# Kernel tuning notes

Hardware: AMD Instinct MI355X
Metric: run time of the kernel (lower is better)

The kernel has to match this reference:

```python
import jax, jax.numpy as jnp
import numpy as np

DIM = 192
HEADS = 4
EPS_LN = 1e-5
EPS_NORM = 1e-12


def _layernorm(x, w, b):
    # x: [b, c, h, w]; normalize over channel dim (equiv to 'b (h w) c' LN over last axis)
    mu = jnp.mean(x, axis=1, keepdims=True)
    var = jnp.mean((x - mu) ** 2, axis=1, keepdims=True)
    return (x - mu) / jnp.sqrt(var + EPS_LN) * w[None, :, None, None] + b[None, :, None, None]


def _conv1x1(x, w):
    # w: [out_c, in_c]
    return jnp.einsum('bchw,oc->bohw', x, w)


def _dwconv3x3(x, w):
    # w: [c, 1, 3, 3], depthwise (groups = c), padding 1
    return jax.lax.conv_general_dilated(
        x, w, window_strides=(1, 1), padding='SAME',
        feature_group_count=x.shape[1],
        dimension_numbers=('NCHW', 'OIHW', 'NCHW'))


def _l2norm(x):
    # F.normalize(dim=-1): x / max(||x||_2, eps)
    n = jnp.sqrt(jnp.sum(x * x, axis=-1, keepdims=True))
    return x / jnp.maximum(n, EPS_NORM)


def setup_inputs() -> dict:
    key = jax.random.key(0)
    ks = jax.random.split(key, 10)
    b, c, h, w = 8, DIM, 128, 128
    inp = {
        'xx': jax.random.normal(ks[0], (b, c, h, w), jnp.float32),
        'q_in': jax.random.normal(ks[1], (b, c, h, w), jnp.float32),
        'ln_w': jnp.ones((c,), jnp.float32),
        'ln_b': jnp.zeros((c,), jnp.float32),
        'w_q': jax.random.normal(ks[2], (c, c), jnp.float32) * 0.02,
        'w_k': jax.random.normal(ks[3], (c, c), jnp.float32) * 0.02,
        'w_v': jax.random.normal(ks[4], (c, c), jnp.float32) * 0.02,
        'wd_q': jax.random.normal(ks[5], (c, 1, 3, 3), jnp.float32) * 0.1,
        'wd_k': jax.random.normal(ks[6], (c, 1, 3, 3), jnp.float32) * 0.1,
        'wd_v': jax.random.normal(ks[7], (c, 1, 3, 3), jnp.float32) * 0.1,
        'w_proj': jax.random.normal(ks[8], (c, c), jnp.float32) * 0.02,
        'temperature': jnp.ones((HEADS, 1, 1), jnp.float32),
    }
    return inp


def reference(xx, q_in, ln_w, ln_b, w_q, w_k, w_v, wd_q, wd_k, wd_v, w_proj, temperature):
    b, c, h, w = xx.shape
    hw = h * w
    dh = c // HEADS  # per-head channel dim

    x_n = _layernorm(xx, ln_w, ln_b)
    q_n = _layernorm(q_in, ln_w, ln_b)

    q = _dwconv3x3(_conv1x1(q_n, w_q), wd_q)
    k = _dwconv3x3(_conv1x1(x_n, w_k), wd_k)
    v = _dwconv3x3(_conv1x1(x_n, w_v), wd_v)

    # b (head c) h w -> b head c (h w)
    q = q.reshape(b, HEADS, dh, hw)
    k = k.reshape(b, HEADS, dh, hw)
    v = v.reshape(b, HEADS, dh, hw)

    q = _l2norm(q)
    k = _l2norm(k)

    # channel-channel attention: [b, head, dh, dh]
    attn = jnp.einsum('bhcn,bhdn->bhcd', q, k) * temperature[None]
    attn = jax.nn.softmax(attn, axis=-1)

    out = jnp.einsum('bhcd,bhdn->bhcn', attn, v)  # [b, head, dh, hw]
    out = out.reshape(b, c, h, w)
    out = _conv1x1(out, w_proj) + q_in
    return out
```

## Files before the change

### kernel.cpp

```cpp
#include <hip/hip_runtime.h>
#include <hip/hip_bf16.h>
#include <stdint.h>

#define HWSZ 16384
#define CCH 192
#define NB 8
#define NHEAD 4
#define DHEAD 48

typedef unsigned short u16;
typedef __bf16 bf16x8 __attribute__((ext_vector_type(8)));
typedef float f32x4 __attribute__((ext_vector_type(4)));
typedef short s16x8 __attribute__((ext_vector_type(8)));
typedef short s16x4 __attribute__((ext_vector_type(4)));

__device__ __forceinline__ float b2f(u16 h){
  union { unsigned u; float f; } v; v.u = ((unsigned)h) << 16; return v.f;
}
__device__ __forceinline__ u16 f2b(float f){
  union { float f; unsigned u; } v; v.f = f;
  unsigned r = v.u + 0x7fffu + ((v.u >> 16) & 1u);
  return (u16)(r >> 16);
}

__global__ __launch_bounds__(256) void k_wpack(
    const float* __restrict__ wq, const float* __restrict__ wk,
    const float* __restrict__ wv, u16* __restrict__ o)
{
  int m = blockIdx.x;
  const float* src = (m == 0) ? wq : (m == 1) ? wk : wv;
  u16* dst = o + (size_t)m * CCH * CCH;
  int tid = threadIdx.x;
  #pragma unroll
  for (int i = 0; i < 36; ++i){
    int e = (i * 256 + tid) * 4;
    float4 v = *(const float4*)(src + e);
    s16x4 pk;
    pk[0] = (short)f2b(v.x); pk[1] = (short)f2b(v.y);
    pk[2] = (short)f2b(v.z); pk[3] = (short)f2b(v.w);
    *(s16x4*)(dst + e) = pk;
  }
}

__global__ __launch_bounds__(256) void k_stats(
    const float* __restrict__ xx, const float* __restrict__ q_in,
    float* __restrict__ st)
{
  int tid = threadIdx.x;
  int px  = blockIdx.x * 256 + tid;
  int b   = blockIdx.y, sel = blockIdx.z;
  const float* in = (sel ? q_in : xx) + (size_t)b * CCH * HWSZ + px;
  float s0 = 0.f, s1 = 0.f, q0 = 0.f, q1 = 0.f;
  #pragma unroll 8
  for (int c = 0; c < CCH; c += 2){
    float va = in[(size_t)c * HWSZ];
    float vb = in[(size_t)(c + 1) * HWSZ];
    s0 += va; q0 += va * va;
    s1 += vb; q1 += vb * vb;
  }
  float s = s0 + s1, ss = q0 + q1;
  float mu  = s * (1.f / CCH);
  float var = ss * (1.f / CCH) - mu * mu;
  float2 o = make_float2(mu, rsqrtf(var + 1e-5f));
  *(float2*)(st + ((size_t)(sel * NB + b) * HWSZ + px) * 2) = o;
}

__global__ __launch_bounds__(512) void k_conv(
    const float* __restrict__ xx, const float* __restrict__ q_in,
    const float* __restrict__ St,
    const float* __restrict__ lnw, const float* __restrict__ lnb,
    const u16* __restrict__ Wb,
    u16* __restrict__ Ok, u16* __restrict__ Ov, u16* __restrict__ Oq)
{
  __shared__ u16 lnT[96 * 264];
  int tid = threadIdx.x;
  int b   = blockIdx.y;
  int z   = blockIdx.z;
  int p0  = blockIdx.x * 128;

  {
    const float* xb = (z ? q_in : xx) + (size_t)b * CCH * HWSZ + p0;
    const float* sb = St + ((size_t)(z * NB + b) * HWSZ + p0) * 2;
    #pragma unroll
    for (int i = 0; i < 6; ++i){
      int e = i * 512 + tid;
      int c = e >> 4, ns = (e & 15) * 8;
      float4 v0 = *(const float4*)(xb + (size_t)c * HWSZ + ns);
      float4 v1 = *(const float4*)(xb + (size_t)c * HWSZ + ns + 4);
      float4 t0 = *(const float4*)(sb + ns * 2);
      float4 t1 = *(const float4*)(sb + ns * 2 + 4);
      float4 t2 = *(const float4*)(sb + ns * 2 + 8);
      float4 t3 = *(const float4*)(sb + ns * 2 + 12);
      float lw_ = lnw[c], lb_ = lnb[c];
      s16x8 pk;
      pk[0] = (short)f2b((v0.x - t0.x) * t0.y * lw_ + lb_);
      pk[1] = (short)f2b((v0.y - t0.z) * t0.w * lw_ + lb_);
      pk[2] = (short)f2b((v0.z - t1.x) * t1.y * lw_ + lb_);
      pk[3] = (short)f2b((v0.w - t1.z) * t1.w * lw_ + lb_);
      pk[4] = (short)f2b((v1.x - t2.x) * t2.y * lw_ + lb_);
      pk[5] = (short)f2b((v1.y - t2.z) * t2.w * lw_ + lb_);
      pk[6] = (short)f2b((v1.z - t3.x) * t3.y * lw_ + lb_);
      pk[7] = (short)f2b((v1.w - t3.z) * t3.w * lw_ + lb_);
      int kb   = c >> 5, kr = c & 31;
      int tile = (kr >> 2) & 1;
      int mr   = ((kr >> 3) << 2) | (kr & 3);
      int ti   = (kb * 8 + (ns >> 4)) * 2 + tile;
      *(s16x8*)(&lnT[ti * 264 + mr * 16 + (ns & 15)]) = pk;
    }
  }
  __syncthreads();

  int lane = tid & 63, wid = tid >> 6;
  int quad = lane >> 4, r = lane & 15;
  int mq = wid & 3;
  int wm = mq * 48;
  const u16* W;
  u16* O;
  if (z == 0){
    W = Wb + (size_t)((wid >> 2) + 1) * CCH * CCH;
    O = (wid >> 2) ? Ov : Ok;
  } else {
    W = Wb;
    O = Oq;
  }
  int nt  = z ? 1 : 2;
  int nhS = z ? (wid >> 2) : 0;
  const u16* A0 = W + (size_t)wm * CCH;
  unsigned lvb0 = (unsigned)(uintptr_t)(&lnT[0]) + 2u * (unsigned)(r + quad * 64);
  size_t ob = (size_t)b * CCH * HWSZ;

  for (int t = 0; t < nt; ++t){
    int nh = z ? nhS : t;
    f32x4 acc[3][4] = {};
    bf16x8 aC[3], aN[3];
    #pragma unroll
    for (int i = 0; i < 3; ++i)
      aC[i] = *(const bf16x8*)(A0 + (size_t)(i * 16 + r) * CCH + quad * 8);
    #pragma unroll
    for (int kb = 0; kb < 6; ++kb){
      s16x4 lo[4], hi[4];
      #pragma unroll
      for (int j = 0; j < 4; ++j){
        unsigned a = lvb0 + (unsigned)(kb * 8448 + (nh * 4 + j) * 1056);
        asm volatile("ds_read_b64_tr_b16 %0, %1" : "=&v"(lo[j]) : "v"(a));
        asm volatile("ds_read_b64_tr_b16 %0, %1 offset:528" : "=&v"(hi[j]) : "v"(a));
      }
      if (kb < 5){
        #pragma unroll
        for (int i = 0; i < 3; ++i)
          aN[i] = *(const bf16x8*)(A0 + (size_t)(i * 16 + r) * CCH + (kb + 1) * 32 + quad * 8);
      }
      asm volatile("s_waitcnt lgkmcnt(0)" ::: "memory");
      __builtin_amdgcn_sched_barrier(0);
      #pragma unroll
      for (int j = 0; j < 4; ++j){
        union { s16x8 s; bf16x8 b; } u;
        u.s = __builtin_shufflevector(lo[j], hi[j], 0, 1, 2, 3, 4, 5, 6, 7);
        #pragma unroll
        for (int i = 0; i < 3; ++i)
          acc[i][j] = __builtin_amdgcn_mfma_f32_16x16x32_bf16(aC[i], u.b, acc[i][j], 0, 0, 0);
      }
      #pragma unroll
      for (int i = 0; i < 3; ++i) aC[i] = aN[i];
    }
    #pragma unroll
    for (int i = 0; i < 3; ++i){
      #pragma unroll
      for (int rg = 0; rg < 4; ++rg){
        int o = wm + i * 16 + quad * 4 + rg;
        size_t rowb = ob + (size_t)o * HWSZ;
        #pragma unroll
        for (int j = 0; j < 4; ++j)
          O[rowb + p0 + nh * 64 + j * 16 + r] = f2b(acc[i][j][rg]);
      }
    }
  }
}

__global__ __launch_bounds__(256) void k_dw3(
    const float* __restrict__ wq, const float* __restrict__ wk,
    const float* __restrict__ wv,
    u16* __restrict__ bq, u16* __restrict__ bk, u16* __restrict__ bv,
    float* __restrict__ ssq_q, float* __restrict__ ssq_k)
{
  int tid = threadIdx.x;
  int bc  = blockIdx.x;
  int z   = blockIdx.y;
  int c   = bc % CCH;
  const float* wd = (z == 0) ? wq : (z == 1) ? wk : wv;
  u16* buf = (z == 0) ? bq : (z == 1) ? bk : bv;
  float w[9];
  #pragma unroll
  for (int t = 0; t < 9; ++t) w[t] = wd[c * 9 + t];
  u16* p = buf + (size_t)bc * HWSZ;

  int xseg = tid & 15, ygrp = tid >> 4;
  int x0 = xseg * 8, y0 = ygrp * 8;

  s16x8 zz = {0,0,0,0,0,0,0,0};
  s16x8 raw[10];
  #pragma unroll
  for (int rr = 0; rr < 10; ++rr){
    int yy = y0 - 1 + rr;
    raw[rr] = (yy >= 0 && yy < 128) ? *(const s16x8*)(p + yy * 128 + x0) : zz;
  }
  __syncthreads();

  float cf[10][8];
  float lf[10], rgt[10];
  #pragma unroll
  for (int rr = 0; rr < 10; ++rr){
    #pragma unroll
    for (int j = 0; j < 8; ++j) cf[rr][j] = b2f((u16)raw[rr][j]);
    float l  = __shfl_up(cf[rr][7], 1);
    float rr_ = __shfl_down(cf[rr][0], 1);
    lf[rr]  = (xseg > 0)  ? l   : 0.f;
    rgt[rr] = (xseg < 15) ? rr_ : 0.f;
  }

  float ss = 0.f;
  #pragma unroll
  for (int k = 0; k < 8; ++k){
    float acc[8] = {0.f,0.f,0.f,0.f,0.f,0.f,0.f,0.f};
    #pragma unroll
    for (int dy = 0; dy < 3; ++dy){
      int rr = k + dy;
      float wl = w[dy * 3], wc = w[dy * 3 + 1], wr = w[dy * 3 + 2];
      acc[0] += wl * lf[rr] + wc * cf[rr][0] + wr * cf[rr][1];
      #pragma unroll
      for (int j = 1; j < 7; ++j)
        acc[j] += wl * cf[rr][j - 1] + wc * cf[rr][j] + wr * cf[rr][j + 1];
      acc[7] += wl * cf[rr][6] + wc * cf[rr][7] + wr * rgt[rr];
    }
    s16x8 pk;
    #pragma unroll
    for (int j = 0; j < 8; ++j){
      pk[j] = (short)f2b(acc[j]);
      ss += acc[j] * acc[j];
    }
    *(s16x8*)(p + (y0 + k) * 128 + x0) = pk;
  }

  if (z < 2){
    #pragma unroll
    for (int m = 32; m > 0; m >>= 1) ss += __shfl_xor(ss, m);
    if ((tid & 63) == 0) atomicAdd(&((z == 0) ? ssq_q : ssq_k)[bc], ss);
  }
}

__global__ void k_gram(const u16* __restrict__ q, const u16* __restrict__ k,
                       float* __restrict__ G)
{
  __shared__ float gs[4 * 48 * 49];
  int tid = threadIdx.x;
  int chunk = blockIdx.x;
  int h = blockIdx.y, b = blockIdx.z;
  int lane = tid & 63, w = tid >> 6;
  int quad = lane >> 4, r = lane & 15;
  int nb = chunk * 1024 + w * 256;
  const u16* qb = q + ((size_t)b * CCH + h * DHEAD) * HWSZ;
  const u16* kb = k + ((size_t)b * CCH + h * DHEAD) * HWSZ;
  f32x4 acc[3][3] = {};
  for (int s = 0; s < 8; ++s){
    int kk = nb + s * 32 + quad * 8;
    bf16x8 af[3], bfr[3];
    #pragma unroll
    for (int i = 0; i < 3; ++i){
      af[i]  = *(const bf16x8*)(qb + (size_t)(i * 16 + r) * HWSZ + kk);
      bfr[i] = *(const bf16x8*)(kb + (size_t)(i * 16 + r) * HWSZ + kk);
    }
    #pragma unroll
    for (int i = 0; i < 3; ++i)
      #pragma unroll
      for (int j = 0; j < 3; ++j)
        acc[i][j] = __builtin_amdgcn_mfma_f32_16x16x32_bf16(af[i], bfr[j], acc[i][j], 0, 0, 0);
  }
  float* gw = gs + w * (48 * 49);
  #pragma unroll
  for (int i = 0; i < 3; ++i)
    #pragma unroll
    for (int j = 0; j < 3; ++j)
      #pragma unroll
      for (int rg = 0; rg < 4; ++rg){
        int row = i * 16 + quad * 4 + rg;
        int col = j * 16 + r;
        gw[row * 49 + col] = acc[i][j][rg];
      }
  __syncthreads();
  float* gb = G + (size_t)(b * NHEAD + h) * (DHEAD * DHEAD);
  #pragma unroll
  for (int t = 0; t < 9; ++t){
    int e = t * 256 + tid;
    int row = e / 48, col = e - row * 48;
    int o = row * 49 + col;
    float s = gs[o] + gs[48 * 49 + o] + gs[2 * 48 * 49 + o] + gs[3 * 48 * 49 + o];
    atomicAdd(&gb[e], s);
  }
}

__global__ __launch_bounds__(256) void k_mk(
    const float* __restrict__ G, const float* __restrict__ ssq_q,
    const float* __restrict__ ssq_k, const float* __restrict__ temp,
    const float* __restrict__ wp, u16* __restrict__ Mout)
{
  __shared__ u16 Pt[48 * 72];
  __shared__ u16 wA[192 * 72];
  __shared__ float rks[48];
  int tid = threadIdx.x;
  int h = blockIdx.x, b = blockIdx.y;
  {
    s16x8 z = {};
    #pragma unroll
    for (int i = 0; i < 2; ++i){
      int idx = (i * 256 + tid) * 8;
      if (idx < 48 * 72) *(s16x8*)(&Pt[idx]) = z;
    }
    #pragma unroll
    for (int i = 0; i < 7; ++i){
      int idx = (i * 256 + tid) * 8;
      if (idx < 192 * 72) *(s16x8*)(&wA[idx]) = z;
    }
  }
  if (tid < DHEAD)
    rks[tid] = 1.f / fmaxf(sqrtf(ssq_k[b * CCH + h * DHEAD + tid]), 1e-12f);
  __syncthreads();
  if (tid < DHEAD){
    float rq = temp[h] / fmaxf(sqrtf(ssq_q[b * CCH + h * DHEAD + tid]), 1e-12f);
    const float* gr = G + (size_t)(b * NHEAD + h) * (DHEAD * DHEAD) + tid * DHEAD;
    float a[DHEAD];
    float mx = -1e30f;
    #pragma unroll
    for (int d = 0; d < DHEAD; ++d){
      a[d] = gr[d] * rq * rks[d];
      mx = fmaxf(mx, a[d]);
    }
    float sum = 0.f;
    #pragma unroll
    for (int d = 0; d < DHEAD; ++d){ a[d] = __expf(a[d] - mx); sum += a[d]; }
    float inv = 1.f / sum;
    #pragma unroll
    for (int d = 0; d < DHEAD; ++d) Pt[d * 72 + tid] = f2b(a[d] * inv);
  }
  {
    const float* wb = wp + h * DHEAD;
    #pragma unroll
    for (int i = 0; i < 9; ++i){
      int e = (i * 256 + tid) * 4;
      int row = e / DHEAD, col = e - row * DHEAD;
      float4 v = *(const float4*)(wb + (size_t)row * CCH + col);
      s16x4 pk;
      pk[0] = (short)f2b(v.x); pk[1] = (short)f2b(v.y);
      pk[2] = (short)f2b(v.z); pk[3] = (short)f2b(v.w);
      *(s16x4*)(&wA[row * 72 + col]) = pk;
    }
  }
  __syncthreads();
  int lane = tid & 63, wid = tid >> 6;
  int quad = lane >> 4, r = lane & 15;
  int wm = wid * 48;
  f32x4 acc[3][3] = {};
  #pragma unroll
  for (int ks = 0; ks < 2; ++ks){
    int k0 = ks * 32;
    bf16x8 af[3], bf[3];
    #pragma unroll
    for (int i = 0; i < 3; ++i)
      af[i] = *(const bf16x8*)(&wA[(wm + i * 16 + r) * 72 + k0 + quad * 8]);
    #pragma unroll
    for (int j = 0; j < 3; ++j)
      bf[j] = *(const bf16x8*)(&Pt[(j * 16 + r) * 72 + k0 + quad * 8]);
    #pragma unroll
    for (int i = 0; i < 3; ++i)
      #pragma unroll
      for (int j = 0; j < 3; ++j)
        acc[i][j] = __builtin_amdgcn_mfma_f32_16x16x32_bf16(af[i], bf[j], acc[i][j], 0, 0, 0);
  }
  u16* mb = Mout + (size_t)b * (CCH * CCH) + h * DHEAD;
  #pragma unroll
  for (int i = 0; i < 3; ++i)
    #pragma unroll
    for (int j = 0; j < 3; ++j)
      #pragma unroll
      for (int rg = 0; rg < 4; ++rg){
        int o = wm + i * 16 + quad * 4 + rg;
        int d = j * 16 + r;
        mb[(size_t)o * CCH + d] = f2b(acc[i][j][rg]);
      }
}

__global__ __launch_bounds__(256) void k_gemmv(
    const u16* __restrict__ M, const u16* __restrict__ V,
    float* __restrict__ Out, const float* __restrict__ resid)
{
  __shared__ u16 lA[64 * 200];
  __shared__ u16 lV[96 * 264];
  int tid = threadIdx.x;
  int n0 = blockIdx.x * 128;
  int m0 = blockIdx.y * 64;
  int b  = blockIdx.z;
  {
    const u16* ap = M + (size_t)b * (CCH * CCH) + m0 * CCH;
    #pragma unroll
    for (int i = 0; i < 6; ++i){
      int off = (i * 256 + tid) * 8;
      int row = off / CCH, col = off - row * CCH;
      *(int4*)(&lA[row * 200 + col]) = *(const int4*)(ap + off);
    }
  }
  {
    const u16* vp = V + (size_t)b * CCH * HWSZ + n0;
    #pragma unroll
    for (int i = 0; i < 12; ++i){
      int e = i * 256 + tid;
      int c = e >> 4, ns = (e & 15) * 8;
      int4 v = *(const int4*)(vp + (size_t)c * HWSZ + ns);
      int kb = c >> 5, kr = c & 31;
      int tile = (kr >> 2) & 1;
      int mr = ((kr >> 3) << 2) | (kr & 3);
      int ti = (kb * 8 + (ns >> 4)) * 2 + tile;
      *(int4*)(&lV[ti * 264 + mr * 16 + (ns & 15)]) = v;
    }
  }
  __syncthreads();
  int lane = tid & 63, wid = tid >> 6;
  int quad = lane >> 4, r = lane & 15;
  int wm = (wid >> 1) * 32, wn = (wid & 1) * 64;
  unsigned lvb = (unsigned)(uintptr_t)(&lV[0]) + 2u * (unsigned)(r + quad * 64)
               + (unsigned)((wn >> 4) * 2) * 528u;
  f32x4 acc[2][4] = {};
  #pragma unroll
  for (int kb = 0; kb < 6; ++kb){
    int k0 = kb * 32;
    s16x4 lo[4], hi[4];
    #pragma unroll
    for (int j = 0; j < 4; ++j){
      unsigned a = lvb + (unsigned)kb * 8448u + (unsigned)j * 1056u;
      asm volatile("ds_read_b64_tr_b16 %0, %1" : "=&v"(lo[j]) : "v"(a));
      asm volatile("ds_read_b64_tr_b16 %0, %1 offset:528" : "=&v"(hi[j]) : "v"(a));
    }
    bf16x8 af[2];
    #pragma unroll
    for (int i = 0; i < 2; ++i)
      af[i] = *(const bf16x8*)(&lA[(wm + i * 16 + r) * 200 + k0 + quad * 8]);
    asm volatile("s_waitcnt lgkmcnt(0)" ::: "memory");
    __builtin_amdgcn_sched_barrier(0);
    #pragma unroll
    for (int j = 0; j < 4; ++j){
      union { s16x8 s; bf16x8 b; } u;
      u.s = __builtin_shufflevector(lo[j], hi[j], 0, 1, 2, 3, 4, 5, 6, 7);
      #pragma unroll
      for (int i = 0; i < 2; ++i)
        acc[i][j] = __builtin_amdgcn_mfma_f32_16x16x32_bf16(af[i], u.b, acc[i][j], 0, 0, 0);
    }
  }
  size_t obase = (size_t)b * CCH * HWSZ;
  #pragma unroll
  for (int i = 0; i < 2; ++i){
    #pragma unroll
    for (int rg = 0; rg < 4; ++rg){
      int o = m0 + wm + i * 16 + quad * 4 + rg;
      size_t rowb = obase + (size_t)o * HWSZ;
      #pragma unroll
      for (int j = 0; j < 4; ++j){
        int n = n0 + wn + j * 16 + r;
        Out[rowb + n] = acc[i][j][rg] + resid[rowb + n];
      }
    }
  }
}

extern "C" void kernel_launch(void* const* d_in, const int* in_sizes, int n_in,
                              void* d_out, int out_size, void* d_ws, size_t ws_size,
                              hipStream_t stream)
{
  const float* xx     = (const float*)d_in[0];
  const float* q_in   = (const float*)d_in[1];
  const float* ln_w   = (const float*)d_in[2];
  const float* ln_b   = (const float*)d_in[3];
  const float* w_q    = (const float*)d_in[4];
  const float* w_k    = (const float*)d_in[5];
  const float* w_v    = (const float*)d_in[6];
  const float* wd_q   = (const float*)d_in[7];
  const float* wd_k   = (const float*)d_in[8];
  const float* wd_v   = (const float*)d_in[9];
  const float* w_proj = (const float*)d_in[10];
  const float* temp   = (const float*)d_in[11];

  const size_t SZ = (size_t)NB * CCH * HWSZ;
  u16* B1 = (u16*)d_ws;
  u16* B2 = B1 + SZ;
  u16* B3 = B2 + SZ;
  float* G     = (float*)(B3 + SZ);
  float* ssq_q = G + 32 * DHEAD * DHEAD;
  float* ssq_k = ssq_q + NB * CCH;
  u16* Mb      = (u16*)(ssq_k + NB * CCH);
  u16* Wb      = Mb + (size_t)NB * CCH * CCH;
  float* Sb    = (float*)(Wb + 3 * CCH * CCH);

  hipMemsetAsync(G, 0, (size_t)(32 * DHEAD * DHEAD + 2 * NB * CCH) * sizeof(float), stream);

  k_stats<<<dim3(64, NB, 2), 256, 0, stream>>>(xx, q_in, Sb);
  k_wpack<<<3, 256, 0, stream>>>(w_q, w_k, w_v, Wb);
  k_conv<<<dim3(128, NB, 2), 512, 0, stream>>>(
      xx, q_in, Sb, ln_w, ln_b, Wb, B2, B1, B3);
  k_dw3<<<dim3(NB * CCH, 3), 256, 0, stream>>>(wd_q, wd_k, wd_v,
                                               B3, B2, B1, ssq_q, ssq_k);
  k_gram<<<dim3(16, NHEAD, NB), 256, 0, stream>>>(B3, B2, G);
  k_mk<<<dim3(NHEAD, NB), 256, 0, stream>>>(G, ssq_q, ssq_k, temp, w_proj, Mb);
  k_gemmv<<<dim3(128, 3, NB), 256, 0, stream>>>(Mb, B1, (float*)d_out, q_in);
}
```

Measured before the change: 476.0 us.

## Fuse LayerNorm statistics into 1x1 conv via algebraic mean/rstd correction

Removes the separate stats kernel and its second full read of both inputs. The conv kernel now packs raw activations to bf16, computes per-pixel mean and variance in-block with shuffles and shared memory, and applies the normalisation after the GEMM as rstd*(acc - mu*rowsum(W*gamma)) + W·beta. The LN weights are folded into the packed weights, and their row sums are precomputed in k_wpack. Tiles shrink to 64 pixels with 256-thread blocks. Running the GEMM on unnormalised bf16 inputs risks cancellation error when the mean is large.

```diff
diff --git a/kernel.cpp b/kernel.cpp
--- a/kernel.cpp
+++ b/kernel.cpp
@@ -25,112 +25,116 @@
 
 __global__ __launch_bounds__(256) void k_wpack(
     const float* __restrict__ wq, const float* __restrict__ wk,
-    const float* __restrict__ wv, u16* __restrict__ o)
+    const float* __restrict__ wv,
+    const float* __restrict__ lnw, const float* __restrict__ lnb,
+    u16* __restrict__ o, float* __restrict__ ad)
 {
   int m = blockIdx.x;
   const float* src = (m == 0) ? wq : (m == 1) ? wk : wv;
   u16* dst = o + (size_t)m * CCH * CCH;
+  int t = threadIdx.x;
+  if (t < CCH){
+    const float* row = src + (size_t)t * CCH;
+    float a = 0.f, d = 0.f;
+    for (int c = 0; c < CCH; c += 4){
+      float4 w = *(const float4*)(row + c);
+      float4 g = *(const float4*)(lnw + c);
+      float4 bb = *(const float4*)(lnb + c);
+      u16 p0 = f2b(w.x * g.x), p1 = f2b(w.y * g.y);
+      u16 p2 = f2b(w.z * g.z), p3 = f2b(w.w * g.w);
+      a += b2f(p0) + b2f(p1) + b2f(p2) + b2f(p3);
+      d += w.x * bb.x + w.y * bb.y + w.z * bb.z + w.w * bb.w;
+      s16x4 pk;
+      pk[0] = (short)p0; pk[1] = (short)p1; pk[2] = (short)p2; pk[3] = (short)p3;
+      *(s16x4*)(dst + (size_t)t * CCH + c) = pk;
+    }
+    ad[(m * 2 + 0) * CCH + t] = a;
+    ad[(m * 2 + 1) * CCH + t] = d;
+  }
+}
+
+__global__ __launch_bounds__(256, 4) void k_convf(
+    const float* __restrict__ xx, const float* __restrict__ q_in,
+    const u16* __restrict__ Wb, const float* __restrict__ ad,
+    u16* __restrict__ Ok, u16* __restrict__ Ov, u16* __restrict__ Oq)
+{
+  __shared__ u16 lnT[48 * 264];
+  __shared__ float2 redf[4][64];
+  __shared__ float2 mures[64];
   int tid = threadIdx.x;
-  #pragma unroll
-  for (int i = 0; i < 36; ++i){
-    int e = (i * 256 + tid) * 4;
-    float4 v = *(const float4*)(src + e);
-    s16x4 pk;
-    pk[0] = (short)f2b(v.x); pk[1] = (short)f2b(v.y);
-    pk[2] = (short)f2b(v.z); pk[3] = (short)f2b(v.w);
-    *(s16x4*)(dst + e) = pk;
-  }
-}
-
-__global__ __launch_bounds__(256) void k_stats(
-    const float* __restrict__ xx, const float* __restrict__ q_in,
-    float* __restrict__ st)
-{
-  int tid = threadIdx.x;
-  int px  = blockIdx.x * 256 + tid;
-  int b   = blockIdx.y, sel = blockIdx.z;
-  const float* in = (sel ? q_in : xx) + (size_t)b * CCH * HWSZ + px;
-  float s0 = 0.f, s1 = 0.f, q0 = 0.f, q1 = 0.f;
-  #pragma unroll 8
-  for (int c = 0; c < CCH; c += 2){
-    float va = in[(size_t)c * HWSZ];
-    float vb = in[(size_t)(c + 1) * HWSZ];
-    s0 += va; q0 += va * va;
-    s1 += vb; q1 += vb * vb;
-  }
-  float s = s0 + s1, ss = q0 + q1;
-  float mu  = s * (1.f / CCH);
-  float var = ss * (1.f / CCH) - mu * mu;
-  float2 o = make_float2(mu, rsqrtf(var + 1e-5f));
-  *(float2*)(st + ((size_t)(sel * NB + b) * HWSZ + px) * 2) = o;
-}
-
-__global__ __launch_bounds__(512) void k_conv(
-    const float* __restrict__ xx, const float* __restrict__ q_in,
-    const float* __restrict__ St,
-    const float* __restrict__ lnw, const float* __restrict__ lnb,
-    const u16* __restrict__ Wb,
-    u16* __restrict__ Ok, u16* __restrict__ Ov, u16* __restrict__ Oq)
-{
-  __shared__ u16 lnT[96 * 264];
-  int tid = threadIdx.x;
-  int b   = blockIdx.y;
-  int z   = blockIdx.z;
-  int p0  = blockIdx.x * 128;
-
-  {
-    const float* xb = (z ? q_in : xx) + (size_t)b * CCH * HWSZ + p0;
-    const float* sb = St + ((size_t)(z * NB + b) * HWSZ + p0) * 2;
-    #pragma unroll
-    for (int i = 0; i < 6; ++i){
-      int e = i * 512 + tid;
-      int c = e >> 4, ns = (e & 15) * 8;
-      float4 v0 = *(const float4*)(xb + (size_t)c * HWSZ + ns);
-      float4 v1 = *(const float4*)(xb + (size_t)c * HWSZ + ns + 4);
-      float4 t0 = *(const float4*)(sb + ns * 2);
-      float4 t1 = *(const float4*)(sb + ns * 2 + 4);
-      float4 t2 = *(const float4*)(sb + ns * 2 + 8);
-      float4 t3 = *(const float4*)(sb + ns * 2 + 12);
-      float lw_ = lnw[c], lb_ = lnb[c];
-      s16x8 pk;
-      pk[0] = (short)f2b((v0.x - t0.x) * t0.y * lw_ + lb_);
-      pk[1] = (short)f2b((v0.y - t0.z) * t0.w * lw_ + lb_);
-      pk[2] = (short)f2b((v0.z - t1.x) * t1.y * lw_ + lb_);
-      pk[3] = (short)f2b((v0.w - t1.z) * t1.w * lw_ + lb_);
-      pk[4] = (short)f2b((v1.x - t2.x) * t2.y * lw_ + lb_);
-      pk[5] = (short)f2b((v1.y - t2.z) * t2.w * lw_ + lb_);
-      pk[6] = (short)f2b((v1.z - t3.x) * t3.y * lw_ + lb_);
-      pk[7] = (short)f2b((v1.w - t3.z) * t3.w * lw_ + lb_);
-      int kb   = c >> 5, kr = c & 31;
-      int tile = (kr >> 2) & 1;
-      int mr   = ((kr >> 3) << 2) | (kr & 3);
-      int ti   = (kb * 8 + (ns >> 4)) * 2 + tile;
-      *(s16x8*)(&lnT[ti * 264 + mr * 16 + (ns & 15)]) = pk;
-    }
+  int b = blockIdx.y, z = blockIdx.z;
+  int p0 = blockIdx.x * 64;
+  int grp = tid & 7;
+  int cs  = tid >> 3;
+  int lane = tid & 63, w = tid >> 6;
+
+  const float* xb = (z ? q_in : xx) + (size_t)b * CCH * HWSZ + p0 + grp * 8;
+
+  float4 v[12];
+  #pragma unroll
+  for (int i = 0; i < 6; ++i){
+    v[2 * i]     = *(const float4*)(xb + (size_t)(i * 32 + cs) * HWSZ);
+    v[2 * i + 1] = *(const float4*)(xb + (size_t)(i * 32 + cs) * HWSZ + 4);
+  }
+  float s[8] = {}, ss[8] = {};
+  #pragma unroll
+  for (int i = 0; i < 6; ++i){
+    float e0 = v[2*i].x, e1 = v[2*i].y, e2 = v[2*i].z, e3 = v[2*i].w;
+    float e4 = v[2*i+1].x, e5 = v[2*i+1].y, e6 = v[2*i+1].z, e7 = v[2*i+1].w;
+    s[0] += e0; ss[0] += e0*e0;  s[1] += e1; ss[1] += e1*e1;
+    s[2] += e2; ss[2] += e2*e2;  s[3] += e3; ss[3] += e3*e3;
+    s[4] += e4; ss[4] += e4*e4;  s[5] += e5; ss[5] += e5*e5;
+    s[6] += e6; ss[6] += e6*e6;  s[7] += e7; ss[7] += e7*e7;
+  }
+  #pragma unroll
+  for (int i = 0; i < 6; ++i){
+    s16x8 pk;
+    pk[0] = (short)f2b(v[2*i].x);   pk[1] = (short)f2b(v[2*i].y);
+    pk[2] = (short)f2b(v[2*i].z);   pk[3] = (short)f2b(v[2*i].w);
+    pk[4] = (short)f2b(v[2*i+1].x); pk[5] = (short)f2b(v[2*i+1].y);
+    pk[6] = (short)f2b(v[2*i+1].z); pk[7] = (short)f2b(v[2*i+1].w);
+    int tile = (cs >> 2) & 1;
+    int mr   = ((cs >> 3) << 2) | (cs & 3);
+    int ti   = (i * 4 + (grp >> 1)) * 2 + tile;
+    *(s16x8*)(&lnT[ti * 264 + mr * 16 + (grp & 1) * 8]) = pk;
+  }
+  #pragma unroll
+  for (int m = 8; m <= 32; m <<= 1){
+    #pragma unroll
+    for (int j = 0; j < 8; ++j){
+      s[j]  += __shfl_xor(s[j],  m);
+      ss[j] += __shfl_xor(ss[j], m);
+    }
+  }
+  if (lane < 8){
+    #pragma unroll
+    for (int j = 0; j < 8; ++j)
+      redf[w][lane * 8 + j] = make_float2(s[j], ss[j]);
   }
   __syncthreads();
 
-  int lane = tid & 63, wid = tid >> 6;
+  if (tid < 64){
+    float2 t0 = redf[0][tid], t1 = redf[1][tid];
+    float2 t2 = redf[2][tid], t3 = redf[3][tid];
+    float s_ = t0.x + t1.x + t2.x + t3.x;
+    float q_ = t0.y + t1.y + t2.y + t3.y;
+    float mu = s_ * (1.f / CCH);
+    float var = q_ * (1.f / CCH) - mu * mu;
+    mures[tid] = make_float2(mu, rsqrtf(var + 1e-5f));
+  }
+
   int quad = lane >> 4, r = lane & 15;
-  int mq = wid & 3;
-  int wm = mq * 48;
-  const u16* W;
-  u16* O;
-  if (z == 0){
-    W = Wb + (size_t)((wid >> 2) + 1) * CCH * CCH;
-    O = (wid >> 2) ? Ov : Ok;
-  } else {
-    W = Wb;
-    O = Oq;
-  }
-  int nt  = z ? 1 : 2;
-  int nhS = z ? (wid >> 2) : 0;
-  const u16* A0 = W + (size_t)wm * CCH;
+  int wm = w * 48;
+  int nt = z ? 1 : 2;
+  size_t ob = (size_t)b * CCH * HWSZ;
   unsigned lvb0 = (unsigned)(uintptr_t)(&lnT[0]) + 2u * (unsigned)(r + quad * 64);
-  size_t ob = (size_t)b * CCH * HWSZ;
 
   for (int t = 0; t < nt; ++t){
-    int nh = z ? nhS : t;
+    int mi = z ? 0 : (t + 1);
+    const u16* A0 = Wb + (size_t)mi * CCH * CCH + (size_t)wm * CCH;
+    const float* aA = ad + (mi * 2 + 0) * CCH;
+    const float* dA = ad + (mi * 2 + 1) * CCH;
+    u16* O = z ? Oq : (t ? Ov : Ok);
     f32x4 acc[3][4] = {};
     bf16x8 aC[3], aN[3];
     #pragma unroll
@@ -141,7 +145,7 @@
       s16x4 lo[4], hi[4];
       #pragma unroll
       for (int j = 0; j < 4; ++j){
-        unsigned a = lvb0 + (unsigned)(kb * 8448 + (nh * 4 + j) * 1056);
+        unsigned a = lvb0 + (unsigned)(kb * 4224 + j * 1056);
         asm volatile("ds_read_b64_tr_b16 %0, %1" : "=&v"(lo[j]) : "v"(a));
         asm volatile("ds_read_b64_tr_b16 %0, %1 offset:528" : "=&v"(hi[j]) : "v"(a));
       }
@@ -163,15 +167,19 @@
       #pragma unroll
       for (int i = 0; i < 3; ++i) aC[i] = aN[i];
     }
-    #pragma unroll
-    for (int i = 0; i < 3; ++i){
-      #pragma unroll
-      for (int rg = 0; rg < 4; ++rg){
-        int o = wm + i * 16 + quad * 4 + rg;
-        size_t rowb = ob + (size_t)o * HWSZ;
+    if (t == 0) __syncthreads();
+    #pragma unroll
+    for (int j = 0; j < 4; ++j){
+      int px = j * 16 + r;
+      float2 mr_ = mures[px];
+      #pragma unroll
+      for (int i = 0; i < 3; ++i){
         #pragma unroll
-        for (int j = 0; j < 4; ++j)
-          O[rowb + p0 + nh * 64 + j * 16 + r] = f2b(acc[i][j][rg]);
+        for (int rg = 0; rg < 4; ++rg){
+          int o = wm + i * 16 + quad * 4 + rg;
+          float val = mr_.y * (acc[i][j][rg] - mr_.x * aA[o]) + dA[o];
+          O[ob + (size_t)o * HWSZ + p0 + px] = f2b(val);
+        }
       }
     }
   }
@@ -495,14 +503,13 @@
   float* ssq_k = ssq_q + NB * CCH;
   u16* Mb      = (u16*)(ssq_k + NB * CCH);
   u16* Wb      = Mb + (size_t)NB * CCH * CCH;
-  float* Sb    = (float*)(Wb + 3 * CCH * CCH);
+  float* Ad    = (float*)(Wb + 3 * CCH * CCH);
 
   hipMemsetAsync(G, 0, (size_t)(32 * DHEAD * DHEAD + 2 * NB * CCH) * sizeof(float), stream);
 
-  k_stats<<<dim3(64, NB, 2), 256, 0, stream>>>(xx, q_in, Sb);
-  k_wpack<<<3, 256, 0, stream>>>(w_q, w_k, w_v, Wb);
-  k_conv<<<dim3(128, NB, 2), 512, 0, stream>>>(
-      xx, q_in, Sb, ln_w, ln_b, Wb, B2, B1, B3);
+  k_wpack<<<3, 256, 0, stream>>>(w_q, w_k, w_v, ln_w, ln_b, Wb, Ad);
+  k_convf<<<dim3(256, NB, 2), 256, 0, stream>>>(
+      xx, q_in, Wb, Ad, B2, B1, B3);
   k_dw3<<<dim3(NB * CCH, 3), 256, 0, stream>>>(wd_q, wd_k, wd_v,
                                                B3, B2, B1, ssq_q, ssq_k);
   k_gram<<<dim3(16, NHEAD, NB), 256, 0, stream>>>(B3, B2, G);
```

Result: no change. 482.6 us (+1.4%).
